# Performance work log

Hardware: AMD Instinct MI355X
Metric: run time of the kernel (lower is better)

## Reference

```python
import jax, jax.numpy as jnp
import numpy as np

B, H, E, DFF, K = 4096, 1024, 8, 4096, 2
THRESH = 0.1


def setup_inputs() -> dict:
    key = jax.random.key(0)
    ks = jax.random.split(key, 8)
    g = lambda k, shape, scale: (jax.random.normal(k, shape, jnp.float32) * scale)
    return {
        "x": jax.random.normal(ks[0], (B, H), jnp.float32),
        "gate_w1": g(ks[1], (H, H // 2), 0.03),
        "gate_b1": jnp.zeros((H // 2,), jnp.float32),
        "gate_w2": g(ks[2], (H // 2, E), 0.06),
        "gate_b2": jnp.zeros((E,), jnp.float32),
        "exp_w1": g(ks[3], (E, H, DFF), 0.03),
        "exp_b1": jnp.zeros((E, DFF), jnp.float32),
        "exp_w2": g(ks[4], (E, DFF, H), 0.015),
        "exp_b2": jnp.zeros((E, H), jnp.float32),
        "proj_w": g(ks[5], (E, H, H), 0.03),
        "blend": jnp.asarray(0.0, jnp.float32),
    }


def reference(x, gate_w1, gate_b1, gate_w2, gate_b2,
              exp_w1, exp_b1, exp_w2, exp_b2, proj_w, blend):
    # PathGate: Linear -> SiLU -> Linear, logits (B, E)
    logits = jax.nn.silu(x @ gate_w1 + gate_b1) @ gate_w2 + gate_b2
    # eval mode (training=False): plain softmax (Markov bayes adjustment = 0)
    gate_weights = jax.nn.softmax(logits, axis=-1)

    # top-k selection with firing threshold
    top_vals, top_idx = jax.lax.top_k(gate_weights, K)        # (B, K)
    keep = top_vals > THRESH                                  # (B, K)
    # scatter kept top-k weights back to dense (B, E) dispatch weights
    onehot = jax.nn.one_hot(top_idx, E, dtype=gate_weights.dtype)  # (B, K, E)
    w_full = jnp.sum(jnp.where(keep[..., None], top_vals[..., None], 0.0) * onehot, axis=1)  # (B, E)

    # per-expert MLP + out_proj, weighted combine (loop over fixed E experts)
    combined = jnp.zeros_like(x)
    for e in range(E):
        h = jax.nn.silu(x @ exp_w1[e] + exp_b1[e]) @ exp_w2[e] + exp_b2[e]  # (B, H)
        combined = combined + w_full[:, e:e + 1] * (h @ proj_w[e])

    total_weight = jnp.sum(w_full, axis=-1)                   # (B,)
    fired = total_weight > 0
    safe_tw = jnp.where(fired, total_weight, 1.0)
    combined = jnp.where(fired[:, None], combined / safe_tw[:, None], x)

    alpha = jax.nn.sigmoid(blend)
    output = alpha * combined + (1.0 - alpha) * x
    return output, gate_weights
```

## Files before the change

### kernel.cpp

```cpp
#include <hip/hip_runtime.h>
#include <hip/hip_bf16.h>
#include <cmath>

constexpr int NB = 4096;
constexpr int NH = 1024;
constexpr int NE = 8;
constexpr int NF = 4096;
constexpr int NG = 512;
constexpr float THRESH = 0.1f;
constexpr int PAD_ROWS = 128;
constexpr size_t MAXS = (size_t)2 * NB;
constexpr size_t ROWS = MAXS + PAD_ROWS;


typedef float  f32x4  __attribute__((ext_vector_type(4)));
typedef __bf16 bf16x8 __attribute__((ext_vector_type(8)));
typedef __bf16 bf16x4 __attribute__((ext_vector_type(4)));

typedef __attribute__((address_space(1))) void gvoid_t;
typedef __attribute__((address_space(3))) void svoid_t;

__device__ __forceinline__ void gl_lds16(const void* g, void* l)
{
    __builtin_amdgcn_global_load_lds((gvoid_t*)g, (svoid_t*)l, 16, 0, 0);
}

__device__ __forceinline__ float silu_f(float v) { return v / (1.f + expf(-v)); }

__global__ void k_sentinel(float* out, float code)
{
    if (threadIdx.x == 0 && blockIdx.x == 0) out[0] = code;
}

__global__ __launch_bounds__(256) void k_tconv(
    const float* __restrict__ in, __bf16* __restrict__ out, int R, int C)
{
    __shared__ float t[64][65];
    const int e = blockIdx.z;
    const float* I = in + (size_t)e * R * C;
    __bf16* O = out + (size_t)e * R * C;
    const int r0 = blockIdx.y * 64, c0 = blockIdx.x * 64;
    const int tid = threadIdx.x;
#pragma unroll
    for (int i = 0; i < 16; i++) {
        int idx = tid + i * 256;
        int r = idx >> 6, c = idx & 63;
        t[r][c] = I[(size_t)(r0 + r) * C + c0 + c];
    }
    __syncthreads();
#pragma unroll
    for (int i = 0; i < 16; i++) {
        int idx = tid + i * 256;
        int c = idx >> 6, r = idx & 63;
        O[(size_t)(c0 + c) * R + r0 + r] = (__bf16)t[r][c];
    }
}

__global__ __launch_bounds__(256) void k_gate(
    const float* __restrict__ x, const float* __restrict__ w1,
    const float* __restrict__ b1, float* __restrict__ hidden)
{
    __shared__ float As[16][68];
    __shared__ float Bs[16][64];
    const int tid = threadIdx.x;
    const int r0 = blockIdx.y * 64, c0 = blockIdx.x * 64;
    const int tx = tid & 15, ty = tid >> 4;
    float acc[4][4] = {};
    for (int k0 = 0; k0 < NH; k0 += 16) {
#pragma unroll
        for (int i = 0; i < 4; i++) {
            int e = tid + i * 256;
            int m = e >> 4, kk = e & 15;
            As[kk][m] = x[(size_t)(r0 + m) * NH + k0 + kk];
        }
#pragma unroll
        for (int i = 0; i < 4; i++) {
            int e = tid + i * 256;
            int kk = e >> 6, n = e & 63;
            Bs[kk][n] = w1[(size_t)(k0 + kk) * NG + c0 + n];
        }
        __syncthreads();
#pragma unroll
        for (int kk = 0; kk < 16; kk++) {
            f32x4 a = *(const f32x4*)&As[kk][ty * 4];
            f32x4 b = *(const f32x4*)&Bs[kk][tx * 4];
#pragma unroll
            for (int i = 0; i < 4; i++)
#pragma unroll
                for (int j = 0; j < 4; j++)
                    acc[i][j] = fmaf(a[i], b[j], acc[i][j]);
        }
        __syncthreads();
    }
#pragma unroll
    for (int i = 0; i < 4; i++) {
        int row = r0 + ty * 4 + i;
        f32x4 o;
#pragma unroll
        for (int j = 0; j < 4; j++)
            o[j] = silu_f(acc[i][j] + b1[c0 + tx * 4 + j]);
        *(f32x4*)&hidden[(size_t)row * NG + c0 + tx * 4] = o;
    }
}

__global__ __launch_bounds__(64) void k_router(
    const float* __restrict__ hidden, const float* __restrict__ w2,
    const float* __restrict__ b2, float* __restrict__ gw_out,
    int* __restrict__ count, int* __restrict__ slot_row,
    float* __restrict__ slot_w, float* __restrict__ row_total,
    int* __restrict__ row_fired)
{
    const int r = blockIdx.x;
    const int l = threadIdx.x;
    float pe[NE] = {};
    for (int k = l; k < NG; k += 64) {
        float h = hidden[(size_t)r * NG + k];
        const float* wr = w2 + (size_t)k * NE;
#pragma unroll
        for (int e = 0; e < NE; e++) pe[e] += h * wr[e];
    }
#pragma unroll
    for (int e = 0; e < NE; e++) {
#pragma unroll
        for (int m = 1; m < 64; m <<= 1) pe[e] += __shfl_xor(pe[e], m);
    }
    float logit[NE];
    float mx = -1e30f;
#pragma unroll
    for (int e = 0; e < NE; e++) { logit[e] = pe[e] + b2[e]; mx = fmaxf(mx, logit[e]); }
    float w[NE], s = 0.f;
#pragma unroll
    for (int e = 0; e < NE; e++) { w[e] = expf(logit[e] - mx); s += w[e]; }
    float inv = 1.f / s;
#pragma unroll
    for (int e = 0; e < NE; e++) w[e] *= inv;
    if (l < NE) gw_out[(size_t)r * NE + l] = w[l];

    int i1 = 0; float v1 = w[0];
#pragma unroll
    for (int e = 1; e < NE; e++) if (w[e] > v1) { v1 = w[e]; i1 = e; }
    int i2 = -1; float v2 = -1.f;
#pragma unroll
    for (int e = 0; e < NE; e++) if (e != i1 && w[e] > v2) { v2 = w[e]; i2 = e; }

    bool k1 = v1 > THRESH, k2 = v2 > THRESH;
    float total = (k1 ? v1 : 0.f) + (k2 ? v2 : 0.f);
    if (l == 0) {
        row_total[r] = total;
        row_fired[r] = (total > 0.f) ? 1 : 0;
        if (k1) { int p = atomicAdd(&count[i1], 1); slot_row[i1 * NB + p] = r; slot_w[i1 * NB + p] = v1; }
        if (k2) { int p = atomicAdd(&count[i2], 1); slot_row[i2 * NB + p] = r; slot_w[i2 * NB + p] = v2; }
    }
}

__global__ void k_offsets(const int* __restrict__ count, int* __restrict__ offs)
{
    if (threadIdx.x == 0 && blockIdx.x == 0) {
        int s = 0;
        for (int e = 0; e < NE; e++) { offs[e] = s; s += count[e]; }
    }
}

__global__ __launch_bounds__(256) void k_xc(
    const float* __restrict__ x, const int* __restrict__ count,
    const int* __restrict__ offs, const int* __restrict__ slot_row,
    __bf16* __restrict__ Xc)
{
    const int s = blockIdx.x;
    int e = 0;
#pragma unroll
    for (int i = 1; i < NE; i++) if (s >= offs[i]) e = i;
    if (s >= offs[NE - 1] + count[NE - 1]) return;
    const int r = slot_row[e * NB + (s - offs[e])];
    const float* src = x + (size_t)r * NH;
    __bf16* dst = Xc + (size_t)s * NH;
    const int t = threadIdx.x;
    f32x4 v = *(const f32x4*)(src + t * 4);
    bf16x4 o;
#pragma unroll
    for (int j = 0; j < 4; j++) o[j] = (__bf16)v[j];
    *(bf16x4*)(dst + t * 4) = o;
}

template<int ACT, int OM>
__global__ __launch_bounds__(256) void k_gemm2(
    const __bf16* __restrict__ A, int lda,
    const __bf16* __restrict__ Wt, size_t wstride,
    const float* __restrict__ bias, int bstride,
    __bf16* __restrict__ outB, float* __restrict__ outF,
    int N, int Kd, int X,
    const int* __restrict__ count, const int* __restrict__ offs,
    const int* __restrict__ slot_row, const float* __restrict__ slot_w)
{
    const int bx = blockIdx.x;
    const int e  = bx / X;
    const int n0 = (bx % X) * 128;
    const int cnt = count[e];
    const int row0 = blockIdx.y * 128;
    if (row0 >= cnt) return;
    const int off = offs[e];
    const __bf16* W = Wt + (size_t)e * wstride;
    const int tid = threadIdx.x;
    const int lane = tid & 63, wid = tid >> 6;
    const int wm = (wid >> 1) * 64, wn = (wid & 1) * 64;
    const int arow0 = off + row0;

    __shared__ __align__(16) unsigned char sA[128 * 128];
    __shared__ __align__(16) unsigned char sB[128 * 128];

    f32x4 acc[4][4];
#pragma unroll
    for (int mi = 0; mi < 4; mi++)
#pragma unroll
        for (int ni = 0; ni < 4; ni++)
            acc[mi][ni] = (f32x4){0.f, 0.f, 0.f, 0.f};

    const int sub = lane >> 3;
    const int kcx = (lane & 7) ^ sub;

    for (int k0 = 0; k0 < Kd; k0 += 64) {
#pragma unroll
        for (int i = 0; i < 4; i++) {
            int c = wid * 4 + i;
            int row = c * 8 + sub;
            gl_lds16(A + (size_t)(arow0 + row) * lda + k0 + kcx * 8,
                     sA + c * 1024 + lane * 16);
        }
#pragma unroll
        for (int i = 0; i < 4; i++) {
            int c = wid * 4 + i;
            int n = c * 8 + sub;
            gl_lds16(W + (size_t)(n0 + n) * Kd + k0 + kcx * 8,
                     sB + c * 1024 + lane * 16);
        }
        __syncthreads();
#pragma unroll
        for (int ks = 0; ks < 2; ks++) {
            bf16x8 af[4], bfr[4];
            const int kb = ks * 64 + ((lane >> 4) << 4);
#pragma unroll
            for (int mi = 0; mi < 4; mi++) {
                int row = wm + mi * 16 + (lane & 15);
                af[mi] = *(const bf16x8*)(sA + row * 128 + (kb ^ ((row & 7) << 4)));
            }
#pragma unroll
            for (int ni = 0; ni < 4; ni++) {
                int row = wn + ni * 16 + (lane & 15);
                bfr[ni] = *(const bf16x8*)(sB + row * 128 + (kb ^ ((row & 7) << 4)));
            }
#pragma unroll
            for (int mi = 0; mi < 4; mi++)
#pragma unroll
                for (int ni = 0; ni < 4; ni++)
                    acc[mi][ni] = __builtin_amdgcn_mfma_f32_16x16x32_bf16(
                        af[mi], bfr[ni], acc[mi][ni], 0, 0, 0);
        }
        __syncthreads();
    }

    const int q = lane >> 4, cl = lane & 15;
#pragma unroll
    for (int mi = 0; mi < 4; mi++) {
#pragma unroll
        for (int r = 0; r < 4; r++) {
            int srow = row0 + wm + mi * 16 + q * 4 + r;
            if (srow >= cnt) continue;
            if (OM == 0) {
#pragma unroll
                for (int ni = 0; ni < 4; ni++) {
                    int col = n0 + wn + ni * 16 + cl;
                    float vv = acc[mi][ni][r] + bias[(size_t)e * bstride + col];
                    if (ACT) vv = silu_f(vv);
                    outB[(size_t)(off + srow) * N + col] = (__bf16)vv;
                }
            } else {
                int grow = slot_row[e * NB + srow];
                float wsl = slot_w[e * NB + srow];
#pragma unroll
                for (int ni = 0; ni < 4; ni++) {
                    int col = n0 + wn + ni * 16 + cl;
                    atomicAdd(&outF[(size_t)grow * NH + col], wsl * acc[mi][ni][r]);
                }
            }
        }
    }
}

template<int AK, int ACT, int OM>
__global__ __launch_bounds__(256) void k_gemm1(
    const float* __restrict__ Af32, const __bf16* __restrict__ Abf, int lda,
    const float* __restrict__ Wbase, size_t wstride,
    const float* __restrict__ bias_base, int bias_stride,
    __bf16* __restrict__ outB, float* __restrict__ outF,
    int N, int Kd, int X,
    const int* __restrict__ count, const int* __restrict__ offs,
    const int* __restrict__ slot_row, const float* __restrict__ slot_w)
{
    const int bx = blockIdx.x;
    const int e  = bx / X;
    const int n0 = (bx % X) * 128;
    const int cnt = count[e];
    const int row0 = blockIdx.y * 128;
    if (row0 >= cnt) return;
    const int off = offs[e];
    const float* W = Wbase + (size_t)e * wstride;
    const int tid = threadIdx.x;
    const int lane = tid & 63, wid = tid >> 6;
    const int wm = (wid >> 1) * 64, wn = (wid & 1) * 64;

    __shared__ __align__(16) unsigned char sA[128 * 128];
    __shared__ __align__(16) unsigned char sB[128 * 128];

    f32x4 acc[4][4];
#pragma unroll
    for (int mi = 0; mi < 4; mi++)
#pragma unroll
        for (int ni = 0; ni < 4; ni++)
            acc[mi][ni] = (f32x4){0.f, 0.f, 0.f, 0.f};

    for (int k0 = 0; k0 < Kd; k0 += 64) {
#pragma unroll
        for (int i = 0; i < 4; i++) {
            int idx = tid + i * 256;
            int m = idx >> 3, kg = idx & 7;
            int slot = row0 + m;
            bf16x8 v;
            if (slot < cnt) {
                if (AK == 0) {
                    int ri = slot_row[e * NB + slot];
                    const float* p = Af32 + (size_t)ri * lda + k0 + kg * 8;
                    f32x4 f0 = *(const f32x4*)p;
                    f32x4 f1 = *(const f32x4*)(p + 4);
#pragma unroll
                    for (int j = 0; j < 4; j++) { v[j] = (__bf16)f0[j]; v[4 + j] = (__bf16)f1[j]; }
                } else {
                    v = *(const bf16x8*)(Abf + (size_t)(off + slot) * lda + k0 + kg * 8);
                }
            } else {
#pragma unroll
                for (int j = 0; j < 8; j++) v[j] = (__bf16)0.f;
            }
            *(bf16x8*)(sA + m * 128 + ((kg * 16) ^ ((m & 7) << 4))) = v;
        }
#pragma unroll
        for (int i = 0; i < 4; i++) {
            int kg = (tid >> 6) + ((i & 1) << 2);
            int n  = (tid & 63) + ((i >> 1) << 6);
            bf16x8 v;
#pragma unroll
            for (int kk = 0; kk < 8; kk++)
                v[kk] = (__bf16)W[(size_t)(k0 + kg * 8 + kk) * N + n0 + n];
            *(bf16x8*)(sB + n * 128 + ((kg * 16) ^ ((n & 7) << 4))) = v;
        }
        __syncthreads();
#pragma unroll
        for (int ks = 0; ks < 2; ks++) {
            bf16x8 af[4], bfr[4];
            const int kb = ks * 64 + ((lane >> 4) << 4);
#pragma unroll
            for (int mi = 0; mi < 4; mi++) {
                int row = wm + mi * 16 + (lane & 15);
                af[mi] = *(const bf16x8*)(sA + row * 128 + (kb ^ ((row & 7) << 4)));
            }
#pragma unroll
            for (int ni = 0; ni < 4; ni++) {
                int row = wn + ni * 16 + (lane & 15);
                bfr[ni] = *(const bf16x8*)(sB + row * 128 + (kb ^ ((row & 7) << 4)));
            }
#pragma unroll
            for (int mi = 0; mi < 4; mi++)
#pragma unroll
                for (int ni = 0; ni < 4; ni++)
                    acc[mi][ni] = __builtin_amdgcn_mfma_f32_16x16x32_bf16(
                        af[mi], bfr[ni], acc[mi][ni], 0, 0, 0);
        }
        __syncthreads();
    }

    const int q = lane >> 4, cl = lane & 15;
#pragma unroll
    for (int mi = 0; mi < 4; mi++) {
#pragma unroll
        for (int r = 0; r < 4; r++) {
            int srow = row0 + wm + mi * 16 + q * 4 + r;
            if (srow >= cnt) continue;
            if (OM == 0) {
#pragma unroll
                for (int ni = 0; ni < 4; ni++) {
                    int col = n0 + wn + ni * 16 + cl;
                    float vv = acc[mi][ni][r] + bias_base[(size_t)e * bias_stride + col];
                    if (ACT) vv = silu_f(vv);
                    outB[(size_t)(off + srow) * N + col] = (__bf16)vv;
                }
            } else {
                int grow = slot_row[e * NB + srow];
                float wsl = slot_w[e * NB + srow];
#pragma unroll
                for (int ni = 0; ni < 4; ni++) {
                    int col = n0 + wn + ni * 16 + cl;
                    atomicAdd(&outF[(size_t)grow * NH + col], wsl * acc[mi][ni][r]);
                }
            }
        }
    }
}

__global__ __launch_bounds__(256) void k_final(
    const float* __restrict__ x,
    const float* __restrict__ row_total, const int* __restrict__ row_fired,
    const float* __restrict__ blend, float* __restrict__ out)
{
    int idx = blockIdx.x * 256 + threadIdx.x;
    int r = idx >> 8;
    int c = (idx & 255) << 2;
    float alpha = 1.f / (1.f + expf(-blend[0]));
    f32x4 cb = *(const f32x4*)(out + (size_t)r * NH + c);
    f32x4 xv = *(const f32x4*)(x + (size_t)r * NH + c);
    int fired = row_fired[r];
    float inv_t = fired ? (1.f / row_total[r]) : 0.f;
    f32x4 o;
#pragma unroll
    for (int j = 0; j < 4; j++)
        o[j] = fired ? (alpha * (cb[j] * inv_t) + (1.f - alpha) * xv[j]) : xv[j];
    *(f32x4*)&out[(size_t)r * NH + c] = o;
}

extern "C" void kernel_launch(void* const* d_in, const int* in_sizes, int n_in,
                              void* d_out, int out_size, void* d_ws, size_t ws_size,
                              hipStream_t stream)
{
    float* out_main = (float*)d_out;
    float* gw_out   = (float*)d_out + (size_t)NB * NH;

    static const long long EXP[11] = {
        (long long)NB * NH, (long long)NH * NG, NG, (long long)NG * NE, NE,
        (long long)NE * NH * NF, (long long)NE * NF,
        (long long)NE * NF * NH, (long long)NE * NH,
        (long long)NE * NH * NH, 1
    };
    bool ok = (n_in == 11);
    if (ok)
        for (int i = 0; i < 11; i++)
            if ((long long)in_sizes[i] != EXP[i]) { ok = false; break; }
    if (!ok) {
        k_sentinel<<<1, 1, 0, stream>>>((float*)d_out, 2000.f + n_in);
        return;
    }

    const float* x    = (const float*)d_in[0];
    const float* gw1  = (const float*)d_in[1];
    const float* gb1  = (const float*)d_in[2];
    const float* gw2  = (const float*)d_in[3];
    const float* gb2  = (const float*)d_in[4];
    const float* ew1  = (const float*)d_in[5];
    const float* eb1  = (const float*)d_in[6];
    const float* ew2  = (const float*)d_in[7];
    const float* eb2  = (const float*)d_in[8];
    const float* pw   = (const float*)d_in[9];
    const float* blnd = (const float*)d_in[10];

    size_t need = 0;
    size_t off_meta   = need;   need += 512;
    size_t off_srow   = need;   need += (size_t)NE * NB * 4;
    size_t off_sw     = need;   need += (size_t)NE * NB * 4;
    size_t off_total  = need;   need += (size_t)NB * 4;
    size_t off_fired  = need;   need += (size_t)NB * 4;
    size_t off_hidden = need;   need += (size_t)NB * NG * 4;
    size_t base = need;

    size_t a_xc  = base;
    size_t a_h1  = a_xc + ROWS * NH * 2;
    size_t a_h2  = a_h1 + ROWS * NF * 2;
    size_t a_w1  = a_h2 + ROWS * NH * 2;
    size_t a_w2  = a_w1 + (size_t)NE * NH * NF * 2;
    size_t a_wp  = a_w2 + (size_t)NE * NF * NH * 2;
    size_t need_A = a_wp + (size_t)NE * NH * NH * 2;

    size_t b_h1 = base;
    size_t b_h2 = b_h1 + MAXS * NF * 2;
    size_t need_B = b_h2 + MAXS * NH * 2;

    char* ws = (char*)d_ws;
    int*   count     = (int*)(ws + off_meta);
    int*   offs      = count + 8;
    int*   slot_row  = (int*)(ws + off_srow);
    float* slot_w    = (float*)(ws + off_sw);
    float* row_total = (float*)(ws + off_total);
    int*   row_fired = (int*)(ws + off_fired);
    float* hidden    = (float*)(ws + off_hidden);

    const bool tierA = (ws_size >= need_A);
    if (!tierA && ws_size < need_B) {
        k_sentinel<<<1, 1, 0, stream>>>((float*)d_out,
                                        1000.f + (float)(ws_size >> 20));
        return;
    }

    hipMemsetAsync(count, 0, 512, stream);
    hipMemsetAsync(out_main, 0, (size_t)NB * NH * 4, stream);

    k_gate<<<dim3(NG / 64, NB / 64), 256, 0, stream>>>(x, gw1, gb1, hidden);
    k_router<<<dim3(NB), 64, 0, stream>>>(hidden, gw2, gb2, gw_out,
                                          count, slot_row, slot_w, row_total, row_fired);
    k_offsets<<<1, 1, 0, stream>>>(count, offs);

    if (tierA) {
        __bf16* Xc  = (__bf16*)(ws + a_xc);
        __bf16* H1  = (__bf16*)(ws + a_h1);
        __bf16* H2  = (__bf16*)(ws + a_h2);
        __bf16* Wt1 = (__bf16*)(ws + a_w1);
        __bf16* Wt2 = (__bf16*)(ws + a_w2);
        __bf16* Wtp = (__bf16*)(ws + a_wp);

        k_tconv<<<dim3(NF / 64, NH / 64, NE), 256, 0, stream>>>(ew1, Wt1, NH, NF);
        k_tconv<<<dim3(NH / 64, NF / 64, NE), 256, 0, stream>>>(ew2, Wt2, NF, NH);
        k_tconv<<<dim3(NH / 64, NH / 64, NE), 256, 0, stream>>>(pw,  Wtp, NH, NH);
        k_xc<<<dim3((int)MAXS), 256, 0, stream>>>(x, count, offs, slot_row, Xc);

        k_gemm2<1, 0><<<dim3(32 * NE, NB / 128), 256, 0, stream>>>(
            Xc, NH, Wt1, (size_t)NH * NF, eb1, NF,
            H1, nullptr, NF, NH, 32, count, offs, slot_row, slot_w);
        k_gemm2<0, 0><<<dim3(8 * NE, NB / 128), 256, 0, stream>>>(
            H1, NF, Wt2, (size_t)NF * NH, eb2, NH,
            H2, nullptr, NH, NF, 8, count, offs, slot_row, slot_w);
        k_gemm2<0, 1><<<dim3(8 * NE, NB / 128), 256, 0, stream>>>(
            H2, NH, Wtp, (size_t)NH * NH, eb2 , 0,
            nullptr, out_main, NH, NH, 8, count, offs, slot_row, slot_w);
    } else {
        __bf16* H1 = (__bf16*)(ws + b_h1);
        __bf16* H2 = (__bf16*)(ws + b_h2);

        k_gemm1<0, 1, 0><<<dim3(32 * NE, NB / 128), 256, 0, stream>>>(
            x, nullptr, NH, ew1, (size_t)NH * NF, eb1, NF,
            H1, nullptr, NF, NH, 32, count, offs, slot_row, slot_w);
        k_gemm1<1, 0, 0><<<dim3(8 * NE, NB / 128), 256, 0, stream>>>(
            nullptr, H1, NF, ew2, (size_t)NF * NH, eb2, NH,
            H2, nullptr, NH, NF, 8, count, offs, slot_row, slot_w);
        k_gemm1<1, 0, 1><<<dim3(8 * NE, NB / 128), 256, 0, stream>>>(
            nullptr, H2, NH, pw, (size_t)NH * NH, eb2 , 0,
            nullptr, out_main, NH, NH, 8, count, offs, slot_row, slot_w);
    }

    k_final<<<dim3(NB * NH / 1024), 256, 0, stream>>>(x, row_total,
                                                      row_fired, blnd, out_main);
}
```

Baseline: 571.8 us.

## Double-buffer LDS tiles in expert GEMM to overlap loads with MFMA

The bf16 expert GEMM kernel now uses two LDS buffers per operand. It issues the async global-to-LDS loads for the next K tile before running the MFMA work on the current tile, so memory latency can hide behind compute. The fallback fp32-weight GEMM path is removed, and the workspace-size check now requires the transposed-weight tier. The cost is twice the LDS per block, which may reduce how many blocks fit on each CU.

Measured after the change: 641.6 us. 1.12x slower.

```diff
diff --git a/kernel.cpp b/kernel.cpp
--- a/kernel.cpp
+++ b/kernel.cpp
@@ -205,8 +205,8 @@
     const int wm = (wid >> 1) * 64, wn = (wid & 1) * 64;
     const int arow0 = off + row0;
 
-    __shared__ __align__(16) unsigned char sA[128 * 128];
-    __shared__ __align__(16) unsigned char sB[128 * 128];
+    __shared__ __align__(16) unsigned char sA[2 * 16384];
+    __shared__ __align__(16) unsigned char sB[2 * 16384];
 
     f32x4 acc[4][4];
 #pragma unroll
@@ -218,22 +218,31 @@
     const int sub = lane >> 3;
     const int kcx = (lane & 7) ^ sub;
 
-    for (int k0 = 0; k0 < Kd; k0 += 64) {
+    auto stage = [&](int buf, int k0) {
 #pragma unroll
         for (int i = 0; i < 4; i++) {
             int c = wid * 4 + i;
             int row = c * 8 + sub;
             gl_lds16(A + (size_t)(arow0 + row) * lda + k0 + kcx * 8,
-                     sA + c * 1024 + lane * 16);
+                     sA + buf * 16384 + c * 1024 + lane * 16);
         }
 #pragma unroll
         for (int i = 0; i < 4; i++) {
             int c = wid * 4 + i;
             int n = c * 8 + sub;
             gl_lds16(W + (size_t)(n0 + n) * Kd + k0 + kcx * 8,
-                     sB + c * 1024 + lane * 16);
-        }
-        __syncthreads();
+                     sB + buf * 16384 + c * 1024 + lane * 16);
+        }
+    };
+
+    const int nt = Kd >> 6;
+    stage(0, 0);
+    __syncthreads();
+
+    for (int t = 0; t < nt; ++t) {
+        if (t + 1 < nt) stage((t + 1) & 1, (t + 1) * 64);
+        const unsigned char* pA = sA + (t & 1) * 16384;
+        const unsigned char* pB = sB + (t & 1) * 16384;
 #pragma unroll
         for (int ks = 0; ks < 2; ks++) {
             bf16x8 af[4], bfr[4];
@@ -241,12 +250,12 @@
 #pragma unroll
             for (int mi = 0; mi < 4; mi++) {
                 int row = wm + mi * 16 + (lane & 15);
-                af[mi] = *(const bf16x8*)(sA + row * 128 + (kb ^ ((row & 7) << 4)));
+                af[mi] = *(const bf16x8*)(pA + row * 128 + (kb ^ ((row & 7) << 4)));
             }
 #pragma unroll
             for (int ni = 0; ni < 4; ni++) {
                 int row = wn + ni * 16 + (lane & 15);
-                bfr[ni] = *(const bf16x8*)(sB + row * 128 + (kb ^ ((row & 7) << 4)));
+                bfr[ni] = *(const bf16x8*)(pB + row * 128 + (kb ^ ((row & 7) << 4)));
             }
 #pragma unroll
             for (int mi = 0; mi < 4; mi++)
@@ -270,125 +279,6 @@
                 for (int ni = 0; ni < 4; ni++) {
                     int col = n0 + wn + ni * 16 + cl;
                     float vv = acc[mi][ni][r] + bias[(size_t)e * bstride + col];
-                    if (ACT) vv = silu_f(vv);
-                    outB[(size_t)(off + srow) * N + col] = (__bf16)vv;
-                }
-            } else {
-                int grow = slot_row[e * NB + srow];
-                float wsl = slot_w[e * NB + srow];
-#pragma unroll
-                for (int ni = 0; ni < 4; ni++) {
-                    int col = n0 + wn + ni * 16 + cl;
-                    atomicAdd(&outF[(size_t)grow * NH + col], wsl * acc[mi][ni][r]);
-                }
-            }
-        }
-    }
-}
-
-template<int AK, int ACT, int OM>
-__global__ __launch_bounds__(256) void k_gemm1(
-    const float* __restrict__ Af32, const __bf16* __restrict__ Abf, int lda,
-    const float* __restrict__ Wbase, size_t wstride,
-    const float* __restrict__ bias_base, int bias_stride,
-    __bf16* __restrict__ outB, float* __restrict__ outF,
-    int N, int Kd, int X,
-    const int* __restrict__ count, const int* __restrict__ offs,
-    const int* __restrict__ slot_row, const float* __restrict__ slot_w)
-{
-    const int bx = blockIdx.x;
-    const int e  = bx / X;
-    const int n0 = (bx % X) * 128;
-    const int cnt = count[e];
-    const int row0 = blockIdx.y * 128;
-    if (row0 >= cnt) return;
-    const int off = offs[e];
-    const float* W = Wbase + (size_t)e * wstride;
-    const int tid = threadIdx.x;
-    const int lane = tid & 63, wid = tid >> 6;
-    const int wm = (wid >> 1) * 64, wn = (wid & 1) * 64;
-
-    __shared__ __align__(16) unsigned char sA[128 * 128];
-    __shared__ __align__(16) unsigned char sB[128 * 128];
-
-    f32x4 acc[4][4];
-#pragma unroll
-    for (int mi = 0; mi < 4; mi++)
-#pragma unroll
-        for (int ni = 0; ni < 4; ni++)
-            acc[mi][ni] = (f32x4){0.f, 0.f, 0.f, 0.f};
-
-    for (int k0 = 0; k0 < Kd; k0 += 64) {
-#pragma unroll
-        for (int i = 0; i < 4; i++) {
-            int idx = tid + i * 256;
-            int m = idx >> 3, kg = idx & 7;
-            int slot = row0 + m;
-            bf16x8 v;
-            if (slot < cnt) {
-                if (AK == 0) {
-                    int ri = slot_row[e * NB + slot];
-                    const float* p = Af32 + (size_t)ri * lda + k0 + kg * 8;
-                    f32x4 f0 = *(const f32x4*)p;
-                    f32x4 f1 = *(const f32x4*)(p + 4);
-#pragma unroll
-                    for (int j = 0; j < 4; j++) { v[j] = (__bf16)f0[j]; v[4 + j] = (__bf16)f1[j]; }
-                } else {
-                    v = *(const bf16x8*)(Abf + (size_t)(off + slot) * lda + k0 + kg * 8);
-                }
-            } else {
-#pragma unroll
-                for (int j = 0; j < 8; j++) v[j] = (__bf16)0.f;
-            }
-            *(bf16x8*)(sA + m * 128 + ((kg * 16) ^ ((m & 7) << 4))) = v;
-        }
-#pragma unroll
-        for (int i = 0; i < 4; i++) {
-            int kg = (tid >> 6) + ((i & 1) << 2);
-            int n  = (tid & 63) + ((i >> 1) << 6);
-            bf16x8 v;
-#pragma unroll
-            for (int kk = 0; kk < 8; kk++)
-                v[kk] = (__bf16)W[(size_t)(k0 + kg * 8 + kk) * N + n0 + n];
-            *(bf16x8*)(sB + n * 128 + ((kg * 16) ^ ((n & 7) << 4))) = v;
-        }
-        __syncthreads();
-#pragma unroll
-        for (int ks = 0; ks < 2; ks++) {
-            bf16x8 af[4], bfr[4];
-            const int kb = ks * 64 + ((lane >> 4) << 4);
-#pragma unroll
-            for (int mi = 0; mi < 4; mi++) {
-                int row = wm + mi * 16 + (lane & 15);
-                af[mi] = *(const bf16x8*)(sA + row * 128 + (kb ^ ((row & 7) << 4)));
-            }
-#pragma unroll
-            for (int ni = 0; ni < 4; ni++) {
-                int row = wn + ni * 16 + (lane & 15);
-                bfr[ni] = *(const bf16x8*)(sB + row * 128 + (kb ^ ((row & 7) << 4)));
-            }
-#pragma unroll
-            for (int mi = 0; mi < 4; mi++)
-#pragma unroll
-                for (int ni = 0; ni < 4; ni++)
-                    acc[mi][ni] = __builtin_amdgcn_mfma_f32_16x16x32_bf16(
-                        af[mi], bfr[ni], acc[mi][ni], 0, 0, 0);
-        }
-        __syncthreads();
-    }
-
-    const int q = lane >> 4, cl = lane & 15;
-#pragma unroll
-    for (int mi = 0; mi < 4; mi++) {
-#pragma unroll
-        for (int r = 0; r < 4; r++) {
-            int srow = row0 + wm + mi * 16 + q * 4 + r;
-            if (srow >= cnt) continue;
-            if (OM == 0) {
-#pragma unroll
-                for (int ni = 0; ni < 4; ni++) {
-                    int col = n0 + wn + ni * 16 + cl;
-                    float vv = acc[mi][ni][r] + bias_base[(size_t)e * bias_stride + col];
                     if (ACT) vv = silu_f(vv);
                     outB[(size_t)(off + srow) * N + col] = (__bf16)vv;
                 }
@@ -466,19 +356,13 @@
     size_t off_total  = need;   need += (size_t)NB * 4;
     size_t off_fired  = need;   need += (size_t)NB * 4;
     size_t off_hidden = need;   need += (size_t)NB * NG * 4;
-    size_t base = need;
-
-    size_t a_xc  = base;
+    size_t a_xc  = need;
     size_t a_h1  = a_xc + ROWS * NH * 2;
     size_t a_h2  = a_h1 + ROWS * NF * 2;
     size_t a_w1  = a_h2 + ROWS * NH * 2;
     size_t a_w2  = a_w1 + (size_t)NE * NH * NF * 2;
     size_t a_wp  = a_w2 + (size_t)NE * NF * NH * 2;
     size_t need_A = a_wp + (size_t)NE * NH * NH * 2;
-
-    size_t b_h1 = base;
-    size_t b_h2 = b_h1 + MAXS * NF * 2;
-    size_t need_B = b_h2 + MAXS * NH * 2;
 
     char* ws = (char*)d_ws;
     int*   count     = (int*)(ws + off_meta);
@@ -489,12 +373,17 @@
     int*   row_fired = (int*)(ws + off_fired);
     float* hidden    = (float*)(ws + off_hidden);
 
-    const bool tierA = (ws_size >= need_A);
-    if (!tierA && ws_size < need_B) {
+    if (ws_size < need_A) {
         k_sentinel<<<1, 1, 0, stream>>>((float*)d_out,
                                         1000.f + (float)(ws_size >> 20));
         return;
     }
+    __bf16* Xc  = (__bf16*)(ws + a_xc);
+    __bf16* H1  = (__bf16*)(ws + a_h1);
+    __bf16* H2  = (__bf16*)(ws + a_h2);
+    __bf16* Wt1 = (__bf16*)(ws + a_w1);
+    __bf16* Wt2 = (__bf16*)(ws + a_w2);
+    __bf16* Wtp = (__bf16*)(ws + a_wp);
 
     hipMemsetAsync(count, 0, 512, stream);
     hipMemsetAsync(out_main, 0, (size_t)NB * NH * 4, stream);
@@ -504,42 +393,20 @@
                                           count, slot_row, slot_w, row_total, row_fired);
     k_offsets<<<1, 1, 0, stream>>>(count, offs);
 
-    if (tierA) {
-        __bf16* Xc  = (__bf16*)(ws + a_xc);
-        __bf16* H1  = (__bf16*)(ws + a_h1);
-        __bf16* H2  = (__bf16*)(ws + a_h2);
-        __bf16* Wt1 = (__bf16*)(ws + a_w1);
-        __bf16* Wt2 = (__bf16*)(ws + a_w2);
-        __bf16* Wtp = (__bf16*)(ws + a_wp);
-
-        k_tconv<<<dim3(NF / 64, NH / 64, NE), 256, 0, stream>>>(ew1, Wt1, NH, NF);
-        k_tconv<<<dim3(NH / 64, NF / 64, NE), 256, 0, stream>>>(ew2, Wt2, NF, NH);
-        k_tconv<<<dim3(NH / 64, NH / 64, NE), 256, 0, stream>>>(pw,  Wtp, NH, NH);
-        k_xc<<<dim3((int)MAXS), 256, 0, stream>>>(x, count, offs, slot_row, Xc);
-
-        k_gemm2<1, 0><<<dim3(32 * NE, NB / 128), 256, 0, stream>>>(
-            Xc, NH, Wt1, (size_t)NH * NF, eb1, NF,
-            H1, nullptr, NF, NH, 32, count, offs, slot_row, slot_w);
-        k_gemm2<0, 0><<<dim3(8 * NE, NB / 128), 256, 0, stream>>>(
-            H1, NF, Wt2, (size_t)NF * NH, eb2, NH,
-            H2, nullptr, NH, NF, 8, count, offs, slot_row, slot_w);
-        k_gemm2<0, 1><<<dim3(8 * NE, NB / 128), 256, 0, stream>>>(
-            H2, NH, Wtp, (size_t)NH * NH, eb2 , 0,
-            nullptr, out_main, NH, NH, 8, count, offs, slot_row, slot_w);
-    } else {
-        __bf16* H1 = (__bf16*)(ws + b_h1);
-        __bf16* H2 = (__bf16*)(ws + b_h2);
-
-        k_gemm1<0, 1, 0><<<dim3(32 * NE, NB / 128), 256, 0, stream>>>(
-            x, nullptr, NH, ew1, (size_t)NH * NF, eb1, NF,
-            H1, nullptr, NF, NH, 32, count, offs, slot_row, slot_w);
-        k_gemm1<1, 0, 0><<<dim3(8 * NE, NB / 128), 256, 0, stream>>>(
-            nullptr, H1, NF, ew2, (size_t)NF * NH, eb2, NH,
-            H2, nullptr, NH, NF, 8, count, offs, slot_row, slot_w);
-        k_gemm1<1, 0, 1><<<dim3(8 * NE, NB / 128), 256, 0, stream>>>(
-            nullptr, H2, NH, pw, (size_t)NH * NH, eb2 , 0,
-            nullptr, out_main, NH, NH, 8, count, offs, slot_row, slot_w);
-    }
+    k_tconv<<<dim3(NF / 64, NH / 64, NE), 256, 0, stream>>>(ew1, Wt1, NH, NF);
+    k_tconv<<<dim3(NH / 64, NF / 64, NE), 256, 0, stream>>>(ew2, Wt2, NF, NH);
+    k_tconv<<<dim3(NH / 64, NH / 64, NE), 256, 0, stream>>>(pw,  Wtp, NH, NH);
+    k_xc<<<dim3((int)MAXS), 256, 0, stream>>>(x, count, offs, slot_row, Xc);
+
+    k_gemm2<1, 0><<<dim3(32 * NE, NB / 128), 256, 0, stream>>>(
+        Xc, NH, Wt1, (size_t)NH * NF, eb1, NF,
+        H1, nullptr, NF, NH, 32, count, offs, slot_row, slot_w);
+    k_gemm2<0, 0><<<dim3(8 * NE, NB / 128), 256, 0, stream>>>(
+        H1, NF, Wt2, (size_t)NF * NH, eb2, NH,
+        H2, nullptr, NH, NF, 8, count, offs, slot_row, slot_w);
+    k_gemm2<0, 1><<<dim3(8 * NE, NB / 128), 256, 0, stream>>>(
+        H2, NH, Wtp, (size_t)NH * NH, eb2 , 0,
+        nullptr, out_main, NH, NH, 8, count, offs, slot_row, slot_w);
 
     k_final<<<dim3(NB * NH / 1024), 256, 0, stream>>>(x, row_total,
                                                       row_fired, blnd, out_main);
```
